# Kernel tuning notes

Measured on AMD Instinct MI355X. Metric: run time of the kernel, lower is better.

Reference implementation:

```python
import jax, jax.numpy as jnp
import numpy as np

M = 262144          # rows of A == prod(out_shape) == 512*512
N = 262144          # cols of A == prod(x.shape)
NNZ = 8388608       # 32 nonzeros per row on average
OUT_SHAPE = (512, 512)


def setup_inputs() -> dict:
    key = jax.random.key(0)
    k1, k2, k3, k4 = jax.random.split(key, 4)
    A_rows = jax.random.randint(k1, (NNZ,), 0, M, dtype=jnp.int32)
    A_cols = jax.random.randint(k2, (NNZ,), 0, N, dtype=jnp.int32)
    A_vals = jax.random.normal(k3, (NNZ,), dtype=jnp.float32)
    x = jax.random.normal(k4, OUT_SHAPE, dtype=jnp.float32)
    return {"x": x, "A_vals": A_vals, "A_rows": A_rows, "A_cols": A_cols}


def reference(x, A_vals, A_rows, A_cols):
    # x.reshape(A.shape[1], 1); torch.sparse.mm(A, x); reshape(out_shape)
    xf = x.reshape(-1)                                   # [N]
    contrib = A_vals * jnp.take(xf, A_cols)              # [NNZ] gather + multiply
    y = jax.ops.segment_sum(contrib, A_rows, num_segments=M)  # scatter-add over rows
    return y.reshape(OUT_SHAPE).astype(jnp.float32)
```

## Files before the change

kernel.cpp:

```cpp
#include <hip/hip_runtime.h>


#define BINS         32
#define ROW_SHIFT    13
#define ROWS_PER_BIN 8192
#define ENT          4096
#define CUR_STRIDE   32
#define SL           16

typedef int   i32x4 __attribute__((ext_vector_type(4)));
typedef float f32x4 __attribute__((ext_vector_type(4)));


__global__ __launch_bounds__(256) void zero_out_kernel(float* __restrict__ y, int n) {
    int i = blockIdx.x * blockDim.x + threadIdx.x;
    if (i < n) y[i] = 0.0f;
}

__global__ __launch_bounds__(256) void spmv_coo_scatter(
    const float* __restrict__ vals, const int* __restrict__ rows,
    const int* __restrict__ cols, const float* __restrict__ x,
    float* __restrict__ y, int nnz)
{
    int i = (blockIdx.x * blockDim.x + threadIdx.x) * 4;
    if (i + 3 < nnz) {
        float4 v = *reinterpret_cast<const float4*>(vals + i);
        int4   r = *reinterpret_cast<const int4*>(rows + i);
        int4   c = *reinterpret_cast<const int4*>(cols + i);
        atomicAdd(&y[r.x], v.x * x[c.x]);
        atomicAdd(&y[r.y], v.y * x[c.y]);
        atomicAdd(&y[r.z], v.z * x[c.z]);
        atomicAdd(&y[r.w], v.w * x[c.w]);
    } else {
        for (; i < nnz; ++i) atomicAdd(&y[rows[i]], vals[i] * x[cols[i]]);
    }
}


__global__ __launch_bounds__(256) void scatter2_kernel(
    const int*   __restrict__ rows, const int* __restrict__ cols,
    const float* __restrict__ vals, const float* __restrict__ x, int nnz,
    unsigned* __restrict__ gcur, unsigned cap,
    unsigned short* __restrict__ okeys, float* __restrict__ ocontrib)
{
    __shared__ unsigned cnt[BINS];
    __shared__ int      dstb[BINS];
    __shared__ unsigned cur2[BINS];
    __shared__ unsigned total_s;
    __shared__ unsigned short skey[ENT];
    __shared__ float          sval[ENT];
    __shared__ unsigned char  sbin[ENT];

    const int t = threadIdx.x;
    if (t < BINS) cnt[t] = 0u;
    __syncthreads();

    const int seg = blockIdx.x * ENT;

    int   rr[16];
    int   cc[16];
    float ff[16];

    if (seg + ENT <= nnz) {
        #pragma unroll
        for (int ch = 0; ch < 4; ++ch) {
            int base = seg + ch * 1024 + t * 4;
            i32x4 r4 = *reinterpret_cast<const i32x4*>(rows + base);
            i32x4 c4 = *reinterpret_cast<const i32x4*>(cols + base);
            f32x4 v4 = *reinterpret_cast<const f32x4*>(vals + base);
            rr[ch*4+0] = r4.x; cc[ch*4+0] = c4.x; ff[ch*4+0] = v4.x;
            rr[ch*4+1] = r4.y; cc[ch*4+1] = c4.y; ff[ch*4+1] = v4.y;
            rr[ch*4+2] = r4.z; cc[ch*4+2] = c4.z; ff[ch*4+2] = v4.z;
            rr[ch*4+3] = r4.w; cc[ch*4+3] = c4.w; ff[ch*4+3] = v4.w;
        }
        #pragma unroll
        for (int j = 0; j < 16; ++j) ff[j] *= x[cc[j]];
    } else {
        #pragma unroll
        for (int ch = 0; ch < 4; ++ch) {
            #pragma unroll
            for (int j = 0; j < 4; ++j) {
                int idx = seg + ch * 1024 + t * 4 + j;
                if (idx < nnz) { rr[ch*4+j] = rows[idx]; cc[ch*4+j] = cols[idx]; ff[ch*4+j] = vals[idx]; }
                else           { rr[ch*4+j] = -1; cc[ch*4+j] = 0; ff[ch*4+j] = 0.0f; }
            }
        }
        #pragma unroll
        for (int j = 0; j < 16; ++j) if (rr[j] >= 0) ff[j] *= x[cc[j]];
    }

    #pragma unroll
    for (int j = 0; j < 16; ++j)
        if (rr[j] >= 0) atomicAdd(&cnt[rr[j] >> ROW_SHIFT], 1u);
    __syncthreads();

    if (t < BINS) {
        unsigned c = cnt[t];
        unsigned resv = atomicAdd(&gcur[t * CUR_STRIDE], c);
        unsigned v = c;
        #pragma unroll
        for (int d = 1; d < BINS; d <<= 1) {
            unsigned o = __shfl_up(v, d, 64);
            if (t >= d) v += o;
        }
        unsigned ls = v - c;
        cur2[t] = ls;
        dstb[t] = (int)resv - (int)ls;
        if (t == BINS - 1) total_s = v;
    }
    __syncthreads();

    #pragma unroll
    for (int j = 0; j < 16; ++j) {
        if (rr[j] >= 0) {
            int b = rr[j] >> ROW_SHIFT;
            unsigned p = atomicAdd(&cur2[b], 1u);
            skey[p] = (unsigned short)(rr[j] & (ROWS_PER_BIN - 1));
            sval[p] = ff[j];
            sbin[p] = (unsigned char)b;
        }
    }
    __syncthreads();

    const unsigned total = total_s;
    for (unsigned i = t; i < total; i += 256) {
        int b = sbin[i];
        unsigned off = (unsigned)(dstb[b] + (int)i);
        if (off < cap) {
            size_t dst = (size_t)b * cap + off;
            okeys[dst]    = skey[i];
            ocontrib[dst] = sval[i];
        }
    }
}

__global__ __launch_bounds__(512) void accum_fused_kernel(
    const unsigned short* __restrict__ okeys, const float* __restrict__ ocontrib,
    const unsigned* __restrict__ gcur, unsigned cap,
    float* __restrict__ partials, unsigned* __restrict__ donec,
    float* __restrict__ y)
{
    __shared__ float acc[ROWS_PER_BIN];
    __shared__ unsigned last_s;
    const int t   = threadIdx.x;
    const int bin = blockIdx.x / SL;
    const int sl  = blockIdx.x - bin * SL;

    float4 z = make_float4(0.f, 0.f, 0.f, 0.f);
    #pragma unroll
    for (int i = 0; i < ROWS_PER_BIN / (512 * 4); ++i)
        *reinterpret_cast<float4*>(&acc[(i * 512 + t) * 4]) = z;
    __syncthreads();

    unsigned count = gcur[bin * CUR_STRIDE];
    if (count > cap) count = cap;
    unsigned chunk = ((count + (unsigned)SL - 1u) / (unsigned)SL + 3u) & ~3u;
    unsigned lo = (unsigned)sl * chunk;
    unsigned hi = lo + chunk; if (hi > count) hi = count;

    const unsigned short* k = okeys    + (size_t)bin * cap;
    const float*          c = ocontrib + (size_t)bin * cap;

    unsigned i = lo + (unsigned)t * 4u;

    for (; i + 6147u < hi; i += 8192u) {
        ushort4 K[4];
        float4  C[4];
        #pragma unroll
        for (int j = 0; j < 4; ++j) K[j] = *reinterpret_cast<const ushort4*>(k + i + (unsigned)j * 2048u);
        #pragma unroll
        for (int j = 0; j < 4; ++j) C[j] = *reinterpret_cast<const float4*>(c + i + (unsigned)j * 2048u);
        #pragma unroll
        for (int j = 0; j < 4; ++j) {
            atomicAdd(&acc[K[j].x], C[j].x);
            atomicAdd(&acc[K[j].y], C[j].y);
            atomicAdd(&acc[K[j].z], C[j].z);
            atomicAdd(&acc[K[j].w], C[j].w);
        }
    }
    for (; i + 3u < hi; i += 2048u) {
        ushort4 k4 = *reinterpret_cast<const ushort4*>(k + i);
        float4  c4 = *reinterpret_cast<const float4*>(c + i);
        atomicAdd(&acc[k4.x], c4.x);
        atomicAdd(&acc[k4.y], c4.y);
        atomicAdd(&acc[k4.z], c4.z);
        atomicAdd(&acc[k4.w], c4.w);
    }
    for (; i < hi; ++i) atomicAdd(&acc[k[i]], c[i]);
    __syncthreads();

    float* p = partials + (size_t)blockIdx.x * ROWS_PER_BIN;
    #pragma unroll
    for (int i2 = 0; i2 < ROWS_PER_BIN / (512 * 4); ++i2) {
        int l = (i2 * 512 + t) * 4;
        *reinterpret_cast<float4*>(p + l) = *reinterpret_cast<const float4*>(&acc[l]);
    }

    __syncthreads();
    if (t == 0) {
        __threadfence();
        unsigned d = __hip_atomic_fetch_add(&donec[bin * CUR_STRIDE], 1u,
                                            __ATOMIC_ACQ_REL, __HIP_MEMORY_SCOPE_AGENT);
        last_s = (d == (unsigned)(SL - 1)) ? 1u : 0u;
    }
    __syncthreads();
    if (!last_s) return;
    __threadfence();

    const float* pb = partials + (size_t)bin * SL * ROWS_PER_BIN;
    float* yb = y + (size_t)bin * ROWS_PER_BIN;
    #pragma unroll
    for (int blk2 = 0; blk2 < ROWS_PER_BIN / (512 * 4); ++blk2) {
        int r0 = (blk2 * 512 + t) * 4;
        float4 s = make_float4(0.f, 0.f, 0.f, 0.f);
        #pragma unroll
        for (int j = 0; j < SL; ++j) {
            float4 v = *reinterpret_cast<const float4*>(pb + (size_t)j * ROWS_PER_BIN + r0);
            s.x += v.x; s.y += v.y; s.z += v.z; s.w += v.w;
        }
        *reinterpret_cast<float4*>(yb + r0) = s;
    }
}

extern "C" void kernel_launch(void* const* d_in, const int* in_sizes, int n_in,
                              void* d_out, int out_size, void* d_ws, size_t ws_size,
                              hipStream_t stream) {
    const float* x    = (const float*)d_in[0];
    const float* vals = (const float*)d_in[1];
    const int*   rows = (const int*)d_in[2];
    const int*   cols = (const int*)d_in[3];
    float* y = (float*)d_out;

    const int nnz  = in_sizes[1];
    const int bins = (out_size + ROWS_PER_BIN - 1) / ROWS_PER_BIN;

    unsigned cap = (unsigned)(nnz / (bins > 0 ? bins : 1)) + 16384u;
    cap = (cap + 3u) & ~3u;

    auto align256 = [](size_t v) { return (v + 255) & ~(size_t)255; };

    size_t off_contrib  = 0;
    size_t off_keys     = align256(off_contrib + (size_t)BINS * cap * 4);
    size_t off_partials = align256(off_keys + (size_t)BINS * cap * 2);
    size_t off_gcur     = align256(off_partials + (size_t)BINS * SL * ROWS_PER_BIN * 4);
    size_t off_done     = off_gcur + (size_t)BINS * CUR_STRIDE * 4;
    size_t need         = align256(off_done + (size_t)BINS * CUR_STRIDE * 4);

    const bool ok = (bins == BINS) && (need <= ws_size) && (nnz > 0) &&
                    (out_size == BINS * ROWS_PER_BIN);

    if (!ok) {
        zero_out_kernel<<<(out_size + 255) / 256, 256, 0, stream>>>(y, out_size);
        spmv_coo_scatter<<<(nnz + 1023) / 1024, 256, 0, stream>>>(vals, rows, cols, x, y, nnz);
        return;
    }

    char* w = (char*)d_ws;
    float*          ocontrib = (float*)(w + off_contrib);
    unsigned short* okeys    = (unsigned short*)(w + off_keys);
    float*          partials = (float*)(w + off_partials);
    unsigned*       gcur     = (unsigned*)(w + off_gcur);
    unsigned*       donec    = (unsigned*)(w + off_done);

    hipMemsetAsync(gcur, 0, (size_t)2 * BINS * CUR_STRIDE * 4, stream);

    scatter2_kernel<<<(nnz + ENT - 1) / ENT, 256, 0, stream>>>(
        rows, cols, vals, x, nnz, gcur, cap, okeys, ocontrib);
    accum_fused_kernel<<<BINS * SL, 512, 0, stream>>>(
        okeys, ocontrib, gcur, cap, partials, donec, y);
}
```

Baseline: 254.8 us.

## Split partial reduction into separate kernel and deepen accumulate unroll

Replaces the last-block-done atomic counter plus in-kernel reduction with a separate reduce kernel that sums the 16 slice partials per row, so no block has to run a serialized tail over a whole bin. It also widens the accumulate loop to 8 in-flight ushort4/float4 loads, separates the x gathers from the multiplies in scatter, and adds min-blocks occupancy hints to launch_bounds. The cost is an extra kernel launch, and the unroll and launch-bounds hints may raise register pressure or cause spills.

Measured after the change: 220.8 us. 1.15x faster.

```diff
diff --git a/kernel.cpp b/kernel.cpp
--- a/kernel.cpp
+++ b/kernel.cpp
@@ -37,7 +37,7 @@
 }
 
 
-__global__ __launch_bounds__(256) void scatter2_kernel(
+__global__ __launch_bounds__(256, 4) void scatter2_kernel(
     const int*   __restrict__ rows, const int* __restrict__ cols,
     const float* __restrict__ vals, const float* __restrict__ x, int nnz,
     unsigned* __restrict__ gcur, unsigned cap,
@@ -73,8 +73,11 @@
             rr[ch*4+2] = r4.z; cc[ch*4+2] = c4.z; ff[ch*4+2] = v4.z;
             rr[ch*4+3] = r4.w; cc[ch*4+3] = c4.w; ff[ch*4+3] = v4.w;
         }
-        #pragma unroll
-        for (int j = 0; j < 16; ++j) ff[j] *= x[cc[j]];
+        float xg[16];
+        #pragma unroll
+        for (int j = 0; j < 16; ++j) xg[j] = x[cc[j]];
+        #pragma unroll
+        for (int j = 0; j < 16; ++j) ff[j] *= xg[j];
     } else {
         #pragma unroll
         for (int ch = 0; ch < 4; ++ch) {
@@ -134,14 +137,12 @@
     }
 }
 
-__global__ __launch_bounds__(512) void accum_fused_kernel(
+__global__ __launch_bounds__(512, 4) void accum2_kernel(
     const unsigned short* __restrict__ okeys, const float* __restrict__ ocontrib,
     const unsigned* __restrict__ gcur, unsigned cap,
-    float* __restrict__ partials, unsigned* __restrict__ donec,
-    float* __restrict__ y)
+    float* __restrict__ partials)
 {
     __shared__ float acc[ROWS_PER_BIN];
-    __shared__ unsigned last_s;
     const int t   = threadIdx.x;
     const int bin = blockIdx.x / SL;
     const int sl  = blockIdx.x - bin * SL;
@@ -163,15 +164,15 @@
 
     unsigned i = lo + (unsigned)t * 4u;
 
-    for (; i + 6147u < hi; i += 8192u) {
-        ushort4 K[4];
-        float4  C[4];
-        #pragma unroll
-        for (int j = 0; j < 4; ++j) K[j] = *reinterpret_cast<const ushort4*>(k + i + (unsigned)j * 2048u);
-        #pragma unroll
-        for (int j = 0; j < 4; ++j) C[j] = *reinterpret_cast<const float4*>(c + i + (unsigned)j * 2048u);
-        #pragma unroll
-        for (int j = 0; j < 4; ++j) {
+    for (; i + 14339u < hi; i += 16384u) {
+        ushort4 K[8];
+        float4  C[8];
+        #pragma unroll
+        for (int j = 0; j < 8; ++j) K[j] = *reinterpret_cast<const ushort4*>(k + i + (unsigned)j * 2048u);
+        #pragma unroll
+        for (int j = 0; j < 8; ++j) C[j] = *reinterpret_cast<const float4*>(c + i + (unsigned)j * 2048u);
+        #pragma unroll
+        for (int j = 0; j < 8; ++j) {
             atomicAdd(&acc[K[j].x], C[j].x);
             atomicAdd(&acc[K[j].y], C[j].y);
             atomicAdd(&acc[K[j].z], C[j].z);
@@ -195,31 +196,22 @@
         int l = (i2 * 512 + t) * 4;
         *reinterpret_cast<float4*>(p + l) = *reinterpret_cast<const float4*>(&acc[l]);
     }
-
-    __syncthreads();
-    if (t == 0) {
-        __threadfence();
-        unsigned d = __hip_atomic_fetch_add(&donec[bin * CUR_STRIDE], 1u,
-                                            __ATOMIC_ACQ_REL, __HIP_MEMORY_SCOPE_AGENT);
-        last_s = (d == (unsigned)(SL - 1)) ? 1u : 0u;
-    }
-    __syncthreads();
-    if (!last_s) return;
-    __threadfence();
-
-    const float* pb = partials + (size_t)bin * SL * ROWS_PER_BIN;
-    float* yb = y + (size_t)bin * ROWS_PER_BIN;
-    #pragma unroll
-    for (int blk2 = 0; blk2 < ROWS_PER_BIN / (512 * 4); ++blk2) {
-        int r0 = (blk2 * 512 + t) * 4;
-        float4 s = make_float4(0.f, 0.f, 0.f, 0.f);
-        #pragma unroll
-        for (int j = 0; j < SL; ++j) {
-            float4 v = *reinterpret_cast<const float4*>(pb + (size_t)j * ROWS_PER_BIN + r0);
-            s.x += v.x; s.y += v.y; s.z += v.z; s.w += v.w;
-        }
-        *reinterpret_cast<float4*>(yb + r0) = s;
-    }
+}
+
+__global__ __launch_bounds__(256) void reduce2_kernel(
+    const float* __restrict__ partials, float* __restrict__ y, int out_size)
+{
+    int r0 = (blockIdx.x * 256 + threadIdx.x) * 4;
+    if (r0 >= out_size) return;
+    int bin = r0 >> ROW_SHIFT, local = r0 & (ROWS_PER_BIN - 1);
+    const float* p = partials + ((size_t)bin * SL) * ROWS_PER_BIN + local;
+    float4 s = make_float4(0.f, 0.f, 0.f, 0.f);
+    #pragma unroll
+    for (int j = 0; j < SL; ++j) {
+        float4 v = *reinterpret_cast<const float4*>(p + (size_t)j * ROWS_PER_BIN);
+        s.x += v.x; s.y += v.y; s.z += v.z; s.w += v.w;
+    }
+    *reinterpret_cast<float4*>(y + r0) = s;
 }
 
 extern "C" void kernel_launch(void* const* d_in, const int* in_sizes, int n_in,
@@ -243,8 +235,7 @@
     size_t off_keys     = align256(off_contrib + (size_t)BINS * cap * 4);
     size_t off_partials = align256(off_keys + (size_t)BINS * cap * 2);
     size_t off_gcur     = align256(off_partials + (size_t)BINS * SL * ROWS_PER_BIN * 4);
-    size_t off_done     = off_gcur + (size_t)BINS * CUR_STRIDE * 4;
-    size_t need         = align256(off_done + (size_t)BINS * CUR_STRIDE * 4);
+    size_t need         = align256(off_gcur + (size_t)BINS * CUR_STRIDE * 4);
 
     const bool ok = (bins == BINS) && (need <= ws_size) && (nnz > 0) &&
                     (out_size == BINS * ROWS_PER_BIN);
@@ -260,12 +251,11 @@
     unsigned short* okeys    = (unsigned short*)(w + off_keys);
     float*          partials = (float*)(w + off_partials);
     unsigned*       gcur     = (unsigned*)(w + off_gcur);
-    unsigned*       donec    = (unsigned*)(w + off_done);
-
-    hipMemsetAsync(gcur, 0, (size_t)2 * BINS * CUR_STRIDE * 4, stream);
+
+    hipMemsetAsync(gcur, 0, (size_t)BINS * CUR_STRIDE * 4, stream);
 
     scatter2_kernel<<<(nnz + ENT - 1) / ENT, 256, 0, stream>>>(
         rows, cols, vals, x, nnz, gcur, cap, okeys, ocontrib);
-    accum_fused_kernel<<<BINS * SL, 512, 0, stream>>>(
-        okeys, ocontrib, gcur, cap, partials, donec, y);
-}
+    accum2_kernel<<<BINS * SL, 512, 0, stream>>>(okeys, ocontrib, gcur, cap, partials);
+    reduce2_kernel<<<(out_size / 4 + 255) / 256, 256, 0, stream>>>(partials, y, out_size);
+}
```
